# Performance work log

Measured on AMD Instinct MI355X. Metric: run time of the kernel, lower is better.

The kernel has to match this reference:

```python
import jax, jax.numpy as jnp
import numpy as np

DIM = 1024
NUM_HEADS = 16
HEAD_DIM = DIM // NUM_HEADS

def setup_inputs() -> dict:
    key = jax.random.key(0)
    ks = jax.random.split(key, 9)
    s = 1.0 / np.sqrt(DIM)
    x = jax.random.normal(ks[0], (4, 1024, DIM), dtype=jnp.float32)
    Wq = jax.random.uniform(ks[1], (DIM, DIM), jnp.float32, -s, s)
    bq = jax.random.uniform(ks[2], (DIM,), jnp.float32, -s, s)
    Wk = jax.random.uniform(ks[3], (DIM, DIM), jnp.float32, -s, s)
    bk = jax.random.uniform(ks[4], (DIM,), jnp.float32, -s, s)
    Wv = jax.random.uniform(ks[5], (DIM, DIM), jnp.float32, -s, s)
    bv = jax.random.uniform(ks[6], (DIM,), jnp.float32, -s, s)
    Wp = jax.random.uniform(ks[7], (DIM, DIM), jnp.float32, -s, s)
    bp = jax.random.uniform(ks[8], (DIM,), jnp.float32, -s, s)
    return {"x": x, "Wq": Wq, "bq": bq, "Wk": Wk, "bk": bk, "Wv": Wv, "bv": bv, "Wp": Wp, "bp": bp}

def reference(x, Wq, bq, Wk, bk, Wv, bv, Wp, bp):
    B, S, D = x.shape
    H, Hd = NUM_HEADS, HEAD_DIM
    # linear projections (torch Linear: y = x @ W^T + b)
    q = (x @ Wq.T + bq).reshape(B, S, H, Hd).transpose(0, 2, 1, 3)  # [B,H,S,Hd]
    k = (x @ Wk.T + bk).reshape(B, S, H, Hd).transpose(0, 2, 1, 3)
    v = (x @ Wv.T + bv).reshape(B, S, H, Hd).transpose(0, 2, 1, 3)
    score = jnp.einsum("bhsd,bhtd->bhst", q, k) / jnp.sqrt(jnp.float32(Hd))
    attn = jax.nn.softmax(score, axis=-1)  # dropout p=0 -> identity
    wa = jnp.einsum("bhst,bhtd->bhsd", attn, v)  # [B,H,S,Hd]
    wa = wa.transpose(0, 2, 1, 3).reshape(B, S, D)
    out = wa @ Wp.T + bp
    return out
```

## Files before the change

kernel.cpp:

```cpp
#include <hip/hip_runtime.h>

typedef unsigned short u16;
typedef unsigned int   u32;
typedef __attribute__((ext_vector_type(8))) short  short8;
typedef __attribute__((ext_vector_type(8))) __bf16 bf16x8;
typedef __attribute__((ext_vector_type(4))) float  f32x4;

__device__ __forceinline__ u16 f2bf(float f){
  u32 u = __builtin_bit_cast(u32, f);
  u32 r = (u + 0x7FFFu + ((u >> 16) & 1u)) >> 16;
  return (u16)r;
}

__device__ __forceinline__ f32x4 mfma16(short8 a, short8 b, f32x4 c){
  return __builtin_amdgcn_mfma_f32_16x16x32_bf16(
      __builtin_bit_cast(bf16x8, a), __builtin_bit_cast(bf16x8, b), c, 0, 0, 0);
}

__device__ __forceinline__ void gl_lds16(const void* g, void* l){
  __builtin_amdgcn_global_load_lds(
      (const __attribute__((address_space(1))) u32*)g,
      (__attribute__((address_space(3))) u32*)l, 16, 0, 0);
}

__global__ void cvt_all(const float* __restrict__ x,  const float* __restrict__ Wq,
                        const float* __restrict__ Wk, const float* __restrict__ Wv,
                        const float* __restrict__ Wp,
                        u16* __restrict__ xb, u16* __restrict__ wqkv,
                        u16* __restrict__ wpb){
  int id = blockIdx.x;
  const float* src; u16* dst; int off;
  if (id < 4096){ src = x; dst = xb; off = id << 8; }
  else {
    int t = id - 4096; int w = t >> 10; int o = t & 1023;
    src = (w==0) ? Wq : (w==1) ? Wk : (w==2) ? Wv : Wp;
    dst = (w==3) ? wpb : wqkv + (size_t)w * 1048576;
    off = o << 8;
  }
  int i = off + threadIdx.x;
  float4 v = reinterpret_cast<const float4*>(src)[i];
  ushort4 u;
  u.x = f2bf(v.x); u.y = f2bf(v.y); u.z = f2bf(v.z); u.w = f2bf(v.w);
  reinterpret_cast<ushort4*>(dst)[i] = u;
}

template<int MODE>
__global__ __launch_bounds__(256) void gemm_bt(
    const u16* __restrict__ A, const u16* __restrict__ B,
    const float* __restrict__ bq, const float* __restrict__ bk,
    const float* __restrict__ bv,
    u16* __restrict__ Oq, u16* __restrict__ Ok, u16* __restrict__ Ovt,
    float* __restrict__ Of, int M, int N, int K)
{
  __shared__ u16 As[2][128*32];
  __shared__ u16 Bs[2][128*32];
  const int tid  = threadIdx.x;
  const int wid  = tid >> 6, lane = tid & 63;

  int gx = gridDim.x;
  int lin = blockIdx.y * gx + blockIdx.x;
  int cpx = (gx * gridDim.y) >> 3;
  int lin2 = (lin & 7) * cpx + (lin >> 3);
  const int m0 = (lin2 / gx) * 128, n0 = (lin2 % gx) * 128;
  const int wr = (wid >> 1) * 64, wc = (wid & 1) * 64;

  f32x4 acc[4][4] = {};
  const int nk = K >> 5;

  auto stage = [&](int buf, int k0){
    #pragma unroll
    for (int ii = 0; ii < 2; ++ii){
      int i = wid * 2 + ii;
      int row = i * 16 + (lane >> 2);
      gl_lds16(A + (size_t)(m0 + row) * K + k0 + (lane & 3) * 8,
               (char*)&As[buf][0] + i * 1024);
    }
    #pragma unroll
    for (int ii = 0; ii < 2; ++ii){
      int i = wid * 2 + ii;
      int row = i * 16 + (lane >> 2);
      gl_lds16(B + (size_t)(n0 + row) * K + k0 + (lane & 3) * 8,
               (char*)&Bs[buf][0] + i * 1024);
    }
  };

  stage(0, 0);
  __syncthreads();
  for (int kt = 0; kt < nk; ++kt){
    int cur = kt & 1;
    if (kt + 1 < nk) stage(cur ^ 1, (kt + 1) << 5);
    short8 a[4], b[4];
    #pragma unroll
    for (int mb = 0; mb < 4; ++mb)
      a[mb] = *(const short8*)&As[cur][(wr + mb*16 + (lane & 15)) * 32 + (lane >> 4) * 8];
    #pragma unroll
    for (int nb = 0; nb < 4; ++nb)
      b[nb] = *(const short8*)&Bs[cur][(wc + nb*16 + (lane & 15)) * 32 + (lane >> 4) * 8];
    #pragma unroll
    for (int mb = 0; mb < 4; ++mb)
      #pragma unroll
      for (int nb = 0; nb < 4; ++nb)
        acc[mb][nb] = mfma16(a[mb], b[nb], acc[mb][nb]);
    __syncthreads();
  }

  const int region = n0 >> 10;
  #pragma unroll
  for (int mb = 0; mb < 4; ++mb){
    int gr0 = m0 + wr + mb * 16 + (lane >> 4) * 4;
    #pragma unroll
    for (int nb = 0; nb < 4; ++nb){
      int gc = n0 + wc + nb * 16 + (lane & 15);
      if (MODE == 1){
        float cbv = bq[gc];
        #pragma unroll
        for (int r = 0; r < 4; ++r)
          Of[(size_t)(gr0 + r) * N + gc] = acc[mb][nb][r] + cbv;
      } else {
        int lc = gc & 1023;
        if (region < 2){
          u16* O = region == 0 ? Oq : Ok;
          float cbv = region == 0 ? bq[lc] : bk[lc];
          #pragma unroll
          for (int r = 0; r < 4; ++r)
            O[(size_t)(gr0 + r) * 1024 + lc] = f2bf(acc[mb][nb][r] + cbv);
        } else {
          float cbv = bv[lc];
          ushort4 o;
          o.x = f2bf(acc[mb][nb][0] + cbv);
          o.y = f2bf(acc[mb][nb][1] + cbv);
          o.z = f2bf(acc[mb][nb][2] + cbv);
          o.w = f2bf(acc[mb][nb][3] + cbv);
          *reinterpret_cast<ushort4*>(&Ovt[(size_t)lc * 4096 + gr0]) = o;
        }
      }
    }
  }
}

__global__ __launch_bounds__(256) void attn_kernel(
    const u16* __restrict__ Q, const u16* __restrict__ Kb,
    const u16* __restrict__ VT, u16* __restrict__ WA)
{
  __shared__ u16 Ks [2][64*64];
  __shared__ u16 VTs[2][64*64];
  __shared__ u16 Ps [4][16*64];

  const int tid = threadIdx.x, wid = tid >> 6, lane = tid & 63;
  const int g = lane >> 4, c = lane & 15;

  const int xcd = blockIdx.x & 7, idx = blockIdx.x >> 3;
  const int bh = xcd * 8 + (idx >> 4), qt = idx & 15;
  const int h = bh & 15, b = bh >> 4;

  const int qr = b*1024 + qt*64 + wid*16 + c;
  short8 qf[2];
  qf[0] = *(const short8*)&Q[(size_t)qr*1024 + h*64 +      g*8];
  qf[1] = *(const short8*)&Q[(size_t)qr*1024 + h*64 + 32 + g*8];

  char* Psw = (char*)&Ps[wid][0];
  float lsum[4] = {0.f,0.f,0.f,0.f};
  f32x4 acc[4] = {};

  auto stage = [&](int buf, int t0){
    #pragma unroll
    for (int ii = 0; ii < 2; ++ii){
      int i  = wid*2 + ii;
      int p0 = i*1024 + lane*16;
      int t  = p0 >> 7;
      int cb = (p0 & 127) ^ ((t & 7) << 4);
      gl_lds16((const char*)(Kb + (size_t)(b*1024 + t0 + t)*1024 + h*64) + cb,
               (char*)&Ks[buf][0] + i*1024);
    }
    #pragma unroll
    for (int ii = 0; ii < 2; ++ii){
      int i  = wid*2 + ii;
      int p0 = i*1024 + lane*16;
      int d  = p0 >> 7;
      int tb = (p0 & 127) ^ ((d & 7) << 4);
      gl_lds16((const char*)(VT + (size_t)(h*64 + d)*4096 + b*1024 + t0) + tb,
               (char*)&VTs[buf][0] + i*1024);
    }
  };

  stage(0, 0);
  __syncthreads();

  for (int kt = 0; kt < 16; ++kt){
    const int cur = kt & 1;
    if (kt < 15) stage(cur ^ 1, (kt + 1) << 6);

    f32x4 sc[4];
    #pragma unroll
    for (int jb = 0; jb < 4; ++jb){
      sc[jb] = f32x4{0.f,0.f,0.f,0.f};
      int trow = jb*16 + c;
      int swz = (trow & 7) << 4;
      #pragma unroll
      for (int kf = 0; kf < 2; ++kf){
        int db = (kf*32 + g*8) * 2;
        short8 kfr = *(const short8*)((const char*)&Ks[cur][0] + trow*128 + (db ^ swz));
        sc[jb] = mfma16(qf[kf], kfr, sc[jb]);
      }
    }

    #pragma unroll
    for (int jb = 0; jb < 4; ++jb){
      int blk = ((jb ^ g) & 3) << 5;
      #pragma unroll
      for (int r = 0; r < 4; ++r){
        float p = __expf(sc[jb][r] * 0.125f);
        lsum[r] += p;
        *(u16*)(Psw + (4*g + r)*128 + blk + c*2) = f2bf(p);
      }
    }
    asm volatile("s_waitcnt lgkmcnt(0)" ::: "memory");

    #pragma unroll
    for (int tf = 0; tf < 2; ++tf){
      int k2  = (tf*32 + g*8) * 2;
      int jbr = k2 >> 5;
      short8 pf = *(const short8*)(Psw + c*128 + ((((jbr ^ (c >> 2)) & 3) << 5) | (k2 & 31)));
      #pragma unroll
      for (int cb = 0; cb < 4; ++cb){
        int d = cb*16 + c;
        short8 vf = *(const short8*)((const char*)&VTs[cur][0] + d*128 + (k2 ^ ((d & 7) << 4)));
        acc[cb] = mfma16(pf, vf, acc[cb]);
      }
    }
    __syncthreads();
  }

  #pragma unroll
  for (int r = 0; r < 4; ++r){
    float v = lsum[r];
    v += __shfl_xor(v, 1); v += __shfl_xor(v, 2);
    v += __shfl_xor(v, 4); v += __shfl_xor(v, 8);
    lsum[r] = 1.0f / v;
  }

  const int m = b*1024 + qt*64 + wid*16 + g*4;
  #pragma unroll
  for (int cb = 0; cb < 4; ++cb){
    int gc = h*64 + cb*16 + c;
    #pragma unroll
    for (int r = 0; r < 4; ++r)
      WA[(size_t)(m + r)*1024 + gc] = f2bf(acc[cb][r] * lsum[r]);
  }
}

extern "C" void kernel_launch(void* const* d_in, const int* in_sizes, int n_in,
                              void* d_out, int out_size, void* d_ws, size_t ws_size,
                              hipStream_t stream)
{
  (void)in_sizes; (void)n_in; (void)out_size; (void)ws_size;
  const float* x  = (const float*)d_in[0];
  const float* Wq = (const float*)d_in[1];
  const float* bq = (const float*)d_in[2];
  const float* Wk = (const float*)d_in[3];
  const float* bk = (const float*)d_in[4];
  const float* Wv = (const float*)d_in[5];
  const float* bv = (const float*)d_in[6];
  const float* Wp = (const float*)d_in[7];
  const float* bp = (const float*)d_in[8];
  float* out = (float*)d_out;

  char* ws = (char*)d_ws;
  const size_t MB = 1u << 20;
  u16* xb   = (u16*)(ws +  0*MB);
  u16* wqkv = (u16*)(ws +  8*MB);
  u16* wpb  = (u16*)(ws + 14*MB);
  u16* Qb   = (u16*)(ws + 16*MB);
  u16* Kb   = (u16*)(ws + 24*MB);
  u16* VTb  = (u16*)(ws + 32*MB);
  u16* WAb  = (u16*)(ws + 40*MB);

  cvt_all<<<8192, 256, 0, stream>>>(x, Wq, Wk, Wv, Wp, xb, wqkv, wpb);

  gemm_bt<0><<<dim3(24,32), 256, 0, stream>>>(xb, wqkv, bq, bk, bv,
                                              Qb, Kb, VTb, nullptr, 4096, 3072, 1024);

  attn_kernel<<<1024, 256, 0, stream>>>(Qb, Kb, VTb, WAb);

  gemm_bt<1><<<dim3(8,32), 256, 0, stream>>>(WAb, wpb, bp, bp, bp,
                                             nullptr, nullptr, nullptr, out, 4096, 1024, 1024);
}
```

Baseline: 184.8 us.

## Load K/V fragments directly from global in attention, fold softmax scale into Q

The attention kernel drops the double-buffered LDS staging of K and V^T and has each lane read its MFMA fragments straight from global memory (relying on L2/cache). The softmax scale times log2(e) is folded into the Q projection epilogue so the inner loop can use exp2f without a multiply. It also adds s_setprio around the MFMA sections and uses native bf16 conversion for P. This removes LDS traffic and shared-memory footprint, which may raise occupancy, but exposes global-load latency with no explicit prefetch.

```diff
diff --git a/kernel.cpp b/kernel.cpp
--- a/kernel.cpp
+++ b/kernel.cpp
@@ -22,6 +22,8 @@
       (const __attribute__((address_space(1))) u32*)g,
       (__attribute__((address_space(3))) u32*)l, 16, 0, 0);
 }
+
+#define CQ 0.18033688011112042f
 
 __global__ void cvt_all(const float* __restrict__ x,  const float* __restrict__ Wq,
                         const float* __restrict__ Wk, const float* __restrict__ Wv,
@@ -121,9 +123,10 @@
         if (region < 2){
           u16* O = region == 0 ? Oq : Ok;
           float cbv = region == 0 ? bq[lc] : bk[lc];
+          float s   = region == 0 ? CQ : 1.0f;
           #pragma unroll
           for (int r = 0; r < 4; ++r)
-            O[(size_t)(gr0 + r) * 1024 + lc] = f2bf(acc[mb][nb][r] + cbv);
+            O[(size_t)(gr0 + r) * 1024 + lc] = f2bf((acc[mb][nb][r] + cbv) * s);
         } else {
           float cbv = bv[lc];
           ushort4 o;
@@ -142,9 +145,7 @@
     const u16* __restrict__ Q, const u16* __restrict__ Kb,
     const u16* __restrict__ VT, u16* __restrict__ WA)
 {
-  __shared__ u16 Ks [2][64*64];
-  __shared__ u16 VTs[2][64*64];
-  __shared__ u16 Ps [4][16*64];
+  __shared__ u16 Ps[4][16*64];
 
   const int tid = threadIdx.x, wid = tid >> 6, lane = tid & 63;
   const int g = lane >> 4, c = lane & 15;
@@ -158,76 +159,55 @@
   qf[0] = *(const short8*)&Q[(size_t)qr*1024 + h*64 +      g*8];
   qf[1] = *(const short8*)&Q[(size_t)qr*1024 + h*64 + 32 + g*8];
 
+  const u16* Kp = Kb + (size_t)(b*1024 + c)*1024 + h*64 + g*8;
+  const u16* Vp = VT + (size_t)(h*64 + c)*4096 + b*1024 + g*8;
+
   char* Psw = (char*)&Ps[wid][0];
   float lsum[4] = {0.f,0.f,0.f,0.f};
   f32x4 acc[4] = {};
 
-  auto stage = [&](int buf, int t0){
-    #pragma unroll
-    for (int ii = 0; ii < 2; ++ii){
-      int i  = wid*2 + ii;
-      int p0 = i*1024 + lane*16;
-      int t  = p0 >> 7;
-      int cb = (p0 & 127) ^ ((t & 7) << 4);
-      gl_lds16((const char*)(Kb + (size_t)(b*1024 + t0 + t)*1024 + h*64) + cb,
-               (char*)&Ks[buf][0] + i*1024);
-    }
-    #pragma unroll
-    for (int ii = 0; ii < 2; ++ii){
-      int i  = wid*2 + ii;
-      int p0 = i*1024 + lane*16;
-      int d  = p0 >> 7;
-      int tb = (p0 & 127) ^ ((d & 7) << 4);
-      gl_lds16((const char*)(VT + (size_t)(h*64 + d)*4096 + b*1024 + t0) + tb,
-               (char*)&VTs[buf][0] + i*1024);
-    }
-  };
-
-  stage(0, 0);
-  __syncthreads();
-
   for (int kt = 0; kt < 16; ++kt){
-    const int cur = kt & 1;
-    if (kt < 15) stage(cur ^ 1, (kt + 1) << 6);
+    const int t0 = kt * 64;
 
     f32x4 sc[4];
+    __builtin_amdgcn_s_setprio(1);
     #pragma unroll
     for (int jb = 0; jb < 4; ++jb){
-      sc[jb] = f32x4{0.f,0.f,0.f,0.f};
-      int trow = jb*16 + c;
-      int swz = (trow & 7) << 4;
-      #pragma unroll
-      for (int kf = 0; kf < 2; ++kf){
-        int db = (kf*32 + g*8) * 2;
-        short8 kfr = *(const short8*)((const char*)&Ks[cur][0] + trow*128 + (db ^ swz));
-        sc[jb] = mfma16(qf[kf], kfr, sc[jb]);
-      }
-    }
+      const u16* kp = Kp + (size_t)(t0 + jb*16)*1024;
+      short8 k0 = *(const short8*)kp;
+      short8 k1 = *(const short8*)(kp + 32);
+      sc[jb] = mfma16(qf[0], k0, f32x4{0.f,0.f,0.f,0.f});
+      sc[jb] = mfma16(qf[1], k1, sc[jb]);
+    }
+    __builtin_amdgcn_s_setprio(0);
 
     #pragma unroll
     for (int jb = 0; jb < 4; ++jb){
       int blk = ((jb ^ g) & 3) << 5;
       #pragma unroll
       for (int r = 0; r < 4; ++r){
-        float p = __expf(sc[jb][r] * 0.125f);
+        float p = exp2f(sc[jb][r]);
         lsum[r] += p;
-        *(u16*)(Psw + (4*g + r)*128 + blk + c*2) = f2bf(p);
+        *(u16*)(Psw + (4*g + r)*128 + blk + c*2) =
+            __builtin_bit_cast(u16, (__bf16)p);
       }
     }
     asm volatile("s_waitcnt lgkmcnt(0)" ::: "memory");
 
+    __builtin_amdgcn_s_setprio(1);
     #pragma unroll
     for (int tf = 0; tf < 2; ++tf){
       int k2  = (tf*32 + g*8) * 2;
       int jbr = k2 >> 5;
       short8 pf = *(const short8*)(Psw + c*128 + ((((jbr ^ (c >> 2)) & 3) << 5) | (k2 & 31)));
+      const u16* vp = Vp + t0 + tf*32;
       #pragma unroll
       for (int cb = 0; cb < 4; ++cb){
-        int d = cb*16 + c;
-        short8 vf = *(const short8*)((const char*)&VTs[cur][0] + d*128 + (k2 ^ ((d & 7) << 4)));
+        short8 vf = *(const short8*)(vp + (size_t)cb*16*4096);
         acc[cb] = mfma16(pf, vf, acc[cb]);
       }
     }
+    __builtin_amdgcn_s_setprio(0);
     __syncthreads();
   }
 
```

After: 263.2 us. 42.5% more time.
